# Performance work log

Measured on AMD Instinct MI355X. Metric: run time of the kernel, lower is better.

## Reference

```python
import jax, jax.numpy as jnp
import numpy as np

N_NODES = 20000
DEG = 6
E = N_NODES * DEG  # 120000 edges == line-graph nodes
D_NODE, D_EDGE = 64, 16
HID, OUT = 128, 128
EPS = 1e-5


def setup_inputs() -> dict:
    key = jax.random.key(0)
    ks = jax.random.split(key, 8)
    rng = np.random.default_rng(0)
    # graph: each node is the source of DEG edges (direction='out' -> index_r = edge_index[0])
    src = np.repeat(np.arange(N_NODES), DEG)
    dst = rng.integers(0, N_NODES, E)
    edge_index = np.stack([src, dst]).astype(np.int64)
    # two_step_index: ordered pairs of distinct edges sharing a source node
    # (bipartite 2-hop, self loops removed), then GATConv add_self_loops re-appends (i,i)
    ii, jj = np.meshgrid(np.arange(DEG), np.arange(DEG), indexing='ij')
    off = ~np.eye(DEG, dtype=bool)
    ii, jj = ii[off], jj[off]  # DEG*(DEG-1) within-group pairs
    base = (np.arange(N_NODES) * DEG)[:, None]
    s2 = np.concatenate([(base + ii[None, :]).ravel(), np.arange(E)])
    d2 = np.concatenate([(base + jj[None, :]).ravel(), np.arange(E)])
    index_2step = np.stack([s2, d2]).astype(np.int64)  # [2, 720000]
    d_in = D_NODE + D_EDGE
    return {
        "edge_attr": jax.random.normal(ks[0], (E, D_EDGE), jnp.float32),
        "node_attr": jax.random.normal(ks[1], (N_NODES, D_NODE), jnp.float32),
        "bn0_g": jnp.ones((d_in,), jnp.float32),
        "bn0_b": jnp.zeros((d_in,), jnp.float32),
        "W1": jax.random.normal(ks[2], (d_in, HID), jnp.float32) / np.sqrt(d_in).astype(np.float32),
        "bn1_g": jnp.ones((HID,), jnp.float32),
        "bn1_b": jnp.zeros((HID,), jnp.float32),
        "Wg": jax.random.normal(ks[3], (HID, OUT), jnp.float32) / np.sqrt(HID).astype(np.float32),
        "att_src": jax.random.normal(ks[4], (OUT,), jnp.float32) * 0.1,
        "att_dst": jax.random.normal(ks[5], (OUT,), jnp.float32) * 0.1,
        "gat_bias": jnp.zeros((OUT,), jnp.float32),
        "bnf_g": jnp.ones((OUT,), jnp.float32),
        "bnf_b": jnp.zeros((OUT,), jnp.float32),
        "edge_index": jnp.asarray(edge_index),
        "index_2step": jnp.asarray(index_2step),
        "num_nodes": N_NODES,
    }


def batch_norm(x, g, b):
    # training-mode BatchNorm1d (biased variance), like the torch module default
    mu = x.mean(0)
    var = x.var(0)
    return (x - mu) * jax.lax.rsqrt(var + EPS) * g + b


def reference(edge_attr, node_attr, bn0_g, bn0_b, W1, bn1_g, bn1_b,
              Wg, att_src, att_dst, gat_bias, bnf_g, bnf_b,
              edge_index, index_2step, num_nodes):
    index_r = edge_index[0]  # [E] source node of each edge (direction='out')
    # h0: per-edge concat of source-node attrs and edge attrs  [E, Dn+De]
    h0 = jnp.concatenate([node_attr[index_r], edge_attr], axis=1)
    # linear encoder: BN -> Linear(no bias) -> BN -> ReLU (dropout p=0)
    h1 = jax.nn.relu(batch_norm(batch_norm(h0, bn0_g, bn0_b) @ W1, bn1_g, bn1_b))
    # --- GATConv (heads=1) on the line graph given by index_2step ---
    E_ = h1.shape[0]
    x = h1 @ Wg                 # [E, OUT]
    a_src = x @ att_src         # [E]
    a_dst = x @ att_dst         # [E]
    s, d = index_2step[0], index_2step[1]
    e = jax.nn.leaky_relu(a_src[s] + a_dst[d], 0.2)          # [E2]
    e = e - jax.ops.segment_max(e, d, num_segments=E_)[d]    # stable edge-softmax
    ex = jnp.exp(e)
    alpha = ex / (jax.ops.segment_sum(ex, d, num_segments=E_)[d] + 1e-16)
    h2 = jax.ops.segment_sum(alpha[:, None] * x[s], d, num_segments=E_) + gat_bias
    # --- global_add_pool keyed by source node id, then final BatchNorm ---
    h3 = jax.ops.segment_sum(h2, index_r, num_segments=num_nodes)  # [N, OUT]
    return batch_norm(h3, bnf_g, bnf_b)
```

## Files before the change

kernel.cpp:

```cpp
#include <hip/hip_runtime.h>

#define N_NODES 20000
#define DEG 6
#define E_EDGES 120000
#define EPS_BN 1e-5f
#define NBLK 1250
#define EB 96
#define NB 16

#define WS_S0SUM 0
#define WS_S0SQ  80
#define WS_BIAS1 160
#define WS_S1SUM 288
#define WS_S1SQ  1312
#define WS_SC1M  2336
#define WS_SH1M  2464
#define WS_FSUM  2592
#define WS_FSQ   2720
#define WS_STATS_FLOATS 2848
#define WS_WT1   2848
#define WS_WGT   8992

typedef float f32x4 __attribute__((ext_vector_type(4)));
typedef short bf16x8 __attribute__((ext_vector_type(8)));

__device__ __forceinline__ unsigned short f2bf(float f) {
  unsigned u = __float_as_uint(f);
  u += 0x7fffu + ((u >> 16) & 1u);
  return (unsigned short)(u >> 16);
}
__device__ __forceinline__ unsigned pack2bf(float a, float b) {
  return (unsigned)f2bf(a) | ((unsigned)f2bf(b) << 16);
}

__global__ __launch_bounds__(256) void k1_bn0_stats(
    const float* __restrict__ node_attr, const float* __restrict__ edge_attr,
    float* __restrict__ ws) {
  __shared__ float red[256];
  const int t = threadIdx.x;
  const int b = blockIdx.x;
  if (b < 128) {
    const int c = t & 63, rl = t >> 6;
    float s = 0.f, q = 0.f;
    for (int row = b * 4 + rl; row < N_NODES; row += 512) {
      float v = node_attr[row * 64 + c];
      s += v; q += v * v;
    }
    red[t] = s;
    __syncthreads();
    if (t < 64) atomicAdd(&ws[WS_S0SUM + t], red[t] + red[t + 64] + red[t + 128] + red[t + 192]);
    __syncthreads();
    red[t] = q;
    __syncthreads();
    if (t < 64) atomicAdd(&ws[WS_S0SQ + t], red[t] + red[t + 64] + red[t + 128] + red[t + 192]);
  } else {
    const int c = t & 15, rl = t >> 4;
    float s = 0.f, q = 0.f;
    for (int row = (b - 128) * 16 + rl; row < E_EDGES; row += 2048) {
      float v = edge_attr[row * 16 + c];
      s += v; q += v * v;
    }
    red[t] = s;
    __syncthreads();
    if (t < 16) {
      float tot = 0.f;
      #pragma unroll
      for (int k = 0; k < 16; ++k) tot += red[t + 16 * k];
      atomicAdd(&ws[WS_S0SUM + 64 + t], tot);
    }
    __syncthreads();
    red[t] = q;
    __syncthreads();
    if (t < 16) {
      float tot = 0.f;
      #pragma unroll
      for (int k = 0; k < 16; ++k) tot += red[t + 16 * k];
      atomicAdd(&ws[WS_S0SQ + 64 + t], tot);
    }
  }
}

__global__ __launch_bounds__(256) void k0_fold(
    const float* __restrict__ W1, const float* __restrict__ Wg,
    const float* __restrict__ bn0_g, const float* __restrict__ bn0_b,
    float* __restrict__ ws) {
  short* wt1 = (short*)(ws + WS_WT1);
  short* wgt = (short*)(ws + WS_WGT);
  const int t0 = blockIdx.x * 256 + threadIdx.x;
  for (int i = t0; i < 128 * 96; i += 32 * 256) {
    int n = i / 96, k = i % 96;
    float v = 0.f;
    if (k < 80) {
      float cnt = (k < 64) ? (float)N_NODES : (float)E_EDGES;
      float mu = ws[WS_S0SUM + k] / cnt;
      float var = ws[WS_S0SQ + k] / cnt - mu * mu;
      v = W1[k * 128 + n] * (bn0_g[k] * rsqrtf(var + EPS_BN));
    }
    wt1[i] = (short)f2bf(v);
  }
  for (int i = t0; i < 128 * 128; i += 32 * 256) {
    int n = i >> 7, k = i & 127;
    wgt[i] = (short)f2bf(Wg[k * 128 + n]);
  }
  if (blockIdx.x == 0 && threadIdx.x < 128) {
    int n = threadIdx.x;
    float s = 0.f;
    for (int k = 0; k < 80; ++k) {
      float cnt = (k < 64) ? (float)N_NODES : (float)E_EDGES;
      float mu = ws[WS_S0SUM + k] / cnt;
      float var = ws[WS_S0SQ + k] / cnt - mu * mu;
      float sc = bn0_g[k] * rsqrtf(var + EPS_BN);
      s += (bn0_b[k] - mu * sc) * W1[k * 128 + n];
    }
    ws[WS_BIAS1 + n] = s;
  }
}

#define STAGE_INPUTS()                                                         \
  {                                                                            \
    int i = t;                                                                 \
    int row = i >> 4, c4 = (i & 15) << 2;                                      \
    float4 v = *(const float4*)&node_attr[(size_t)(g * NB + row) * 64 + c4];   \
    *(uint2*)&n0s[row * 72 + c4] = make_uint2(pack2bf(v.x, v.y), pack2bf(v.z, v.w)); \
  }                                                                            \
  for (int i = t; i < EB * 4; i += 256) {                                      \
    int row = i >> 2, c4 = (i & 3) << 2;                                       \
    float4 v = *(const float4*)&edge_attr[(size_t)(g * EB + row) * 16 + c4];   \
    *(uint2*)&e0s[row * 24 + c4] = make_uint2(pack2bf(v.x, v.y), pack2bf(v.z, v.w)); \
  }                                                                            \
  if (t < 8) zpad[t] = 0;

#define GEMM1_CORE(acc1)                                                       \
  _Pragma("unroll")                                                            \
  for (int ks = 0; ks < 3; ++ks) {                                             \
    bf16x8 bb0 = *(const bf16x8*)&wt1[(Nb + lm) * 96 + ks * 32 + lq * 8];      \
    bf16x8 bb1 = *(const bf16x8*)&wt1[(Nb + 16 + lm) * 96 + ks * 32 + lq * 8]; \
    _Pragma("unroll")                                                          \
    for (int mt = 0; mt < 6; ++mt) {                                           \
      const short* ap;                                                         \
      if (ks < 2) ap = &n0s[rowdiv6[mt] * 72 + ks * 32 + lq * 8];              \
      else ap = (lq < 2) ? &e0s[(mt * 16 + lm) * 24 + lq * 8] : zpad;          \
      bf16x8 a = *(const bf16x8*)ap;                                           \
      acc1[mt][0] = __builtin_amdgcn_mfma_f32_16x16x32_bf16(a, bb0, acc1[mt][0], 0, 0, 0); \
      acc1[mt][1] = __builtin_amdgcn_mfma_f32_16x16x32_bf16(a, bb1, acc1[mt][1], 0, 0, 0); \
    }                                                                          \
  }

__global__ __launch_bounds__(256, 2) void k2_bn1_stats(
    const float* __restrict__ node_attr, const float* __restrict__ edge_attr,
    float* __restrict__ ws) {
  __shared__ __align__(16) short n0s[16 * 72];
  __shared__ __align__(16) short e0s[96 * 24];
  __shared__ __align__(16) short zpad[8];
  const int t = threadIdx.x;
  const int g = blockIdx.x;
  const int l = t & 63, wid = t >> 6;
  const int lm = l & 15, lq = l >> 4;
  const int Nb = wid * 32;
  const short* wt1 = (const short*)(ws + WS_WT1);
  int rowdiv6[6];
  #pragma unroll
  for (int mt = 0; mt < 6; ++mt) rowdiv6[mt] = (mt * 16 + lm) / 6;
  float bias1c[2];
  bias1c[0] = ws[WS_BIAS1 + Nb + lm];
  bias1c[1] = ws[WS_BIAS1 + Nb + 16 + lm];
  STAGE_INPUTS();
  __syncthreads();
  f32x4 acc1[6][2] = {};
  GEMM1_CORE(acc1);
  const int set = g & 7;
  #pragma unroll
  for (int nt = 0; nt < 2; ++nt) {
    float s = 0.f, q = 0.f;
    #pragma unroll
    for (int mt = 0; mt < 6; ++mt)
      #pragma unroll
      for (int r = 0; r < 4; ++r) {
        float v = acc1[mt][nt][r] + bias1c[nt];
        s += v; q += v * v;
      }
    s += __shfl_xor(s, 16); s += __shfl_xor(s, 32);
    q += __shfl_xor(q, 16); q += __shfl_xor(q, 32);
    if (l < 16) {
      int col = Nb + nt * 16 + lm;
      atomicAdd(&ws[WS_S1SUM + set * 128 + col], s);
      atomicAdd(&ws[WS_S1SQ + set * 128 + col], q);
    }
  }
}

__global__ __launch_bounds__(128) void k2b_finalize(
    const float* __restrict__ bn1_g, const float* __restrict__ bn1_b,
    float* __restrict__ ws) {
  const int t = threadIdx.x;
  float s = 0.f, q = 0.f;
  #pragma unroll
  for (int st = 0; st < 8; ++st) {
    s += ws[WS_S1SUM + st * 128 + t];
    q += ws[WS_S1SQ + st * 128 + t];
  }
  const float invE = 1.f / (float)E_EDGES;
  float mu = s * invE;
  float var = q * invE - mu * mu;
  float sc1 = bn1_g[t] * rsqrtf(var + EPS_BN);
  float sh1 = bn1_b[t] - mu * sc1;
  ws[WS_SC1M + t] = sc1;
  ws[WS_SH1M + t] = ws[WS_BIAS1 + t] * sc1 + sh1;
}

__global__ __launch_bounds__(256, 2) void k3_fused(
    const float* __restrict__ node_attr, const float* __restrict__ edge_attr,
    const float* __restrict__ att_src, const float* __restrict__ att_dst,
    const float* __restrict__ gat_bias,
    float* __restrict__ out, float* __restrict__ ws) {
  __shared__ __align__(16) short n0s[16 * 72];
  __shared__ __align__(16) short e0s[96 * 24];
  __shared__ __align__(16) short zpad[8];
  __shared__ __align__(16) short h1s[96 * 136];
  __shared__ float asP[4][96], adP[4][96];
  __shared__ float asS[96], adS[96], wS[96];
  __shared__ float alphaL[96][6];
  __shared__ float h3L[16 * 128];

  const int t = threadIdx.x;
  const int g = blockIdx.x;
  const int l = t & 63, wid = t >> 6;
  const int lm = l & 15, lq = l >> 4;
  const int Nb = wid * 32;
  const short* wt1 = (const short*)(ws + WS_WT1);
  const short* wgt = (const short*)(ws + WS_WGT);
  int rowdiv6[6];
  #pragma unroll
  for (int mt = 0; mt < 6; ++mt) rowdiv6[mt] = (mt * 16 + lm) / 6;
  float sc1c[2], sh1c[2], atS[2], atD[2];
  #pragma unroll
  for (int nt = 0; nt < 2; ++nt) {
    int col = Nb + nt * 16 + lm;
    sc1c[nt] = ws[WS_SC1M + col];
    sh1c[nt] = ws[WS_SH1M + col];
    atS[nt] = att_src[col];
    atD[nt] = att_dst[col];
  }
  #pragma unroll
  for (int j = 0; j < 2; ++j)
    *(f32x4*)&h3L[(t + j * 256) * 4] = (f32x4){0.f, 0.f, 0.f, 0.f};
  STAGE_INPUTS();
  __syncthreads();
  {
    f32x4 acc1[6][2] = {};
    GEMM1_CORE(acc1);
    #pragma unroll
    for (int mt = 0; mt < 6; ++mt)
      #pragma unroll
      for (int nt = 0; nt < 2; ++nt)
        #pragma unroll
        for (int r = 0; r < 4; ++r) {
          int row = mt * 16 + lq * 4 + r;
          int col = Nb + nt * 16 + lm;
          float v = fmaxf(acc1[mt][nt][r] * sc1c[nt] + sh1c[nt], 0.f);
          h1s[row * 136 + col] = (short)f2bf(v);
        }
  }
  __syncthreads();
  f32x4 acc2[6][2] = {};
  #pragma unroll
  for (int ks = 0; ks < 4; ++ks) {
    bf16x8 bb0 = *(const bf16x8*)&wgt[(Nb + lm) * 128 + ks * 32 + lq * 8];
    bf16x8 bb1 = *(const bf16x8*)&wgt[(Nb + 16 + lm) * 128 + ks * 32 + lq * 8];
    #pragma unroll
    for (int mt = 0; mt < 6; ++mt) {
      bf16x8 a = *(const bf16x8*)&h1s[(mt * 16 + lm) * 136 + ks * 32 + lq * 8];
      acc2[mt][0] = __builtin_amdgcn_mfma_f32_16x16x32_bf16(a, bb0, acc2[mt][0], 0, 0, 0);
      acc2[mt][1] = __builtin_amdgcn_mfma_f32_16x16x32_bf16(a, bb1, acc2[mt][1], 0, 0, 0);
    }
  }
  {
    float ps, pd;
    #pragma unroll
    for (int mt = 0; mt < 6; ++mt)
      #pragma unroll
      for (int r = 0; r < 4; ++r) {
        ps = acc2[mt][0][r] * atS[0] + acc2[mt][1][r] * atS[1];
        pd = acc2[mt][0][r] * atD[0] + acc2[mt][1][r] * atD[1];
        #pragma unroll
        for (int off = 1; off < 16; off <<= 1) {
          ps += __shfl_xor(ps, off);
          pd += __shfl_xor(pd, off);
        }
        if (lm == 0) {
          int row = mt * 16 + lq * 4 + r;
          asP[wid][row] = ps;
          adP[wid][row] = pd;
        }
      }
  }
  __syncthreads();
  if (t < 96) {
    asS[t] = asP[0][t] + asP[1][t] + asP[2][t] + asP[3][t];
    adS[t] = adP[0][t] + adP[1][t] + adP[2][t] + adP[3][t];
  }
  __syncthreads();
  if (t < 96) {
    int n = t / 6;
    int nb6 = n * 6;
    float ad = adS[t];
    float s6[6], m = -1e30f;
    #pragma unroll
    for (int i = 0; i < 6; ++i) {
      float s = asS[nb6 + i] + ad;
      s = (s > 0.f) ? s : 0.2f * s;
      s6[i] = s; m = fmaxf(m, s);
    }
    float ssum = 0.f, ex[6];
    #pragma unroll
    for (int i = 0; i < 6; ++i) { ex[i] = __expf(s6[i] - m); ssum += ex[i]; }
    float inv = 1.f / (ssum + 1e-16f);
    #pragma unroll
    for (int i = 0; i < 6; ++i) alphaL[t][i] = ex[i] * inv;
  }
  __syncthreads();
  if (t < 96) {
    int n = t / 6, i = t % 6;
    float w = 0.f;
    #pragma unroll
    for (int j = 0; j < 6; ++j) w += alphaL[n * 6 + j][i];
    wS[t] = w;
  }
  __syncthreads();
  #pragma unroll
  for (int mt = 0; mt < 6; ++mt)
    #pragma unroll
    for (int r = 0; r < 4; ++r) {
      int row = mt * 16 + lq * 4 + r;
      float w = wS[row];
      int nl = row / 6;
      #pragma unroll
      for (int nt = 0; nt < 2; ++nt)
        atomicAdd(&h3L[nl * 128 + Nb + nt * 16 + lm], w * acc2[mt][nt][r]);
    }
  __syncthreads();
  #pragma unroll
  for (int j = 0; j < 2; ++j) {
    int idx = t + j * 256;
    int nslot = idx >> 5, c4 = (idx & 31) << 2;
    f32x4 v = *(f32x4*)&h3L[nslot * 128 + c4];
    const f32x4 gb = *(const f32x4*)&gat_bias[c4];
    v[0] += 6.f * gb[0]; v[1] += 6.f * gb[1];
    v[2] += 6.f * gb[2]; v[3] += 6.f * gb[3];
    *(f32x4*)&out[(size_t)(g * NB + nslot) * 128 + c4] = v;
  }
}

__global__ __launch_bounds__(256) void k4a_stats(
    const float* __restrict__ out, float* __restrict__ ws) {
  __shared__ float red[8][128];
  const int t = threadIdx.x;
  const int c4 = (t & 31) << 2, rl = t >> 5;
  float fs[4] = {0.f, 0.f, 0.f, 0.f}, fq[4] = {0.f, 0.f, 0.f, 0.f};
  for (int r = blockIdx.x * 8 + rl; r < N_NODES; r += 128 * 8) {
    float4 v = *(const float4*)&out[(size_t)r * 128 + c4];
    fs[0] += v.x; fq[0] += v.x * v.x;
    fs[1] += v.y; fq[1] += v.y * v.y;
    fs[2] += v.z; fq[2] += v.z * v.z;
    fs[3] += v.w; fq[3] += v.w * v.w;
  }
  #pragma unroll
  for (int j = 0; j < 4; ++j) red[rl][c4 + j] = fs[j];
  __syncthreads();
  if (t < 128) {
    float s = 0.f;
    #pragma unroll
    for (int k = 0; k < 8; ++k) s += red[k][t];
    atomicAdd(&ws[WS_FSUM + t], s);
  }
  __syncthreads();
  #pragma unroll
  for (int j = 0; j < 4; ++j) red[rl][c4 + j] = fq[j];
  __syncthreads();
  if (t < 128) {
    float s = 0.f;
    #pragma unroll
    for (int k = 0; k < 8; ++k) s += red[k][t];
    atomicAdd(&ws[WS_FSQ + t], s);
  }
}

__global__ __launch_bounds__(256) void k4b_apply(
    float* __restrict__ out, const float* __restrict__ ws,
    const float* __restrict__ bnf_g, const float* __restrict__ bnf_b) {
  int idx4 = blockIdx.x * 256 + threadIdx.x;
  if (idx4 >= N_NODES * 128 / 4) return;
  int c0 = (idx4 & 31) << 2;
  float4 v = ((float4*)out)[idx4];
  float4 fsv = *(const float4*)&ws[WS_FSUM + c0];
  float4 fqv = *(const float4*)&ws[WS_FSQ + c0];
  float4 g4 = *(const float4*)&bnf_g[c0];
  float4 b4 = *(const float4*)&bnf_b[c0];
  const float invN = 1.f / (float)N_NODES;
  float mu, var, sc;
  mu = fsv.x * invN; var = fqv.x * invN - mu * mu; sc = g4.x * rsqrtf(var + EPS_BN);
  v.x = (v.x - mu) * sc + b4.x;
  mu = fsv.y * invN; var = fqv.y * invN - mu * mu; sc = g4.y * rsqrtf(var + EPS_BN);
  v.y = (v.y - mu) * sc + b4.y;
  mu = fsv.z * invN; var = fqv.z * invN - mu * mu; sc = g4.z * rsqrtf(var + EPS_BN);
  v.z = (v.z - mu) * sc + b4.z;
  mu = fsv.w * invN; var = fqv.w * invN - mu * mu; sc = g4.w * rsqrtf(var + EPS_BN);
  v.w = (v.w - mu) * sc + b4.w;
  ((float4*)out)[idx4] = v;
}

extern "C" void kernel_launch(void* const* d_in, const int* in_sizes, int n_in,
                              void* d_out, int out_size, void* d_ws, size_t ws_size,
                              hipStream_t stream) {
  const float* edge_attr = (const float*)d_in[0];
  const float* node_attr = (const float*)d_in[1];
  const float* bn0_g = (const float*)d_in[2];
  const float* bn0_b = (const float*)d_in[3];
  const float* W1    = (const float*)d_in[4];
  const float* bn1_g = (const float*)d_in[5];
  const float* bn1_b = (const float*)d_in[6];
  const float* Wg    = (const float*)d_in[7];
  const float* att_src = (const float*)d_in[8];
  const float* att_dst = (const float*)d_in[9];
  const float* gat_bias = (const float*)d_in[10];
  const float* bnf_g = (const float*)d_in[11];
  const float* bnf_b = (const float*)d_in[12];
  float* ws = (float*)d_ws;
  float* out = (float*)d_out;

  hipMemsetAsync(d_ws, 0, WS_STATS_FLOATS * sizeof(float), stream);
  k1_bn0_stats<<<256, 256, 0, stream>>>(node_attr, edge_attr, ws);
  k0_fold<<<32, 256, 0, stream>>>(W1, Wg, bn0_g, bn0_b, ws);
  k2_bn1_stats<<<NBLK, 256, 0, stream>>>(node_attr, edge_attr, ws);
  k2b_finalize<<<1, 128, 0, stream>>>(bn1_g, bn1_b, ws);
  k3_fused<<<NBLK, 256, 0, stream>>>(node_attr, edge_attr, att_src, att_dst,
                                     gat_bias, out, ws);
  k4a_stats<<<128, 256, 0, stream>>>(out, ws);
  k4b_apply<<<2500, 256, 0, stream>>>(out, ws, bnf_g, bnf_b);
}
```

Measured before the change: 249.8 us.

## Fuse all stages into one persistent kernel with grid-wide barriers

Replaces the seven separate launches (BN0 stats, weight fold, BN1 stats, finalize, fused GAT, final stats, final apply) with a single persistent kernel of 512 blocks that loops over tiles. Stages are separated by a software grid barrier built on atomics. The intent is to remove per-launch overhead and inter-kernel gaps, and to fold the small finalize steps into per-block prologues. In exchange, every block redundantly recomputes the folded bf16 weights and the BN scales. The barrier also relies on all 512 blocks being co-resident, so it can deadlock if occupancy is lower than assumed.

```diff
diff --git a/kernel.cpp b/kernel.cpp
--- a/kernel.cpp
+++ b/kernel.cpp
@@ -4,22 +4,21 @@
 #define DEG 6
 #define E_EDGES 120000
 #define EPS_BN 1e-5f
-#define NBLK 1250
+#define NTILES 1250
 #define EB 96
 #define NB 16
-
-#define WS_S0SUM 0
-#define WS_S0SQ  80
-#define WS_BIAS1 160
-#define WS_S1SUM 288
-#define WS_S1SQ  1312
-#define WS_SC1M  2336
-#define WS_SH1M  2464
-#define WS_FSUM  2592
-#define WS_FSQ   2720
-#define WS_STATS_FLOATS 2848
-#define WS_WT1   2848
-#define WS_WGT   8992
+#define GRID 512
+
+#define WS_BAR   0
+#define WS_S0SUM 8
+#define WS_S0SQ  88
+#define WS_S1SUM 168
+#define WS_S1SQ  1192
+#define WS_FSUM  2216
+#define WS_FSQ   3240
+#define WS_STATS_FLOATS 4264
+#define WS_WT1   4264
+#define WS_WGT   10408
 
 typedef float f32x4 __attribute__((ext_vector_type(4)));
 typedef short bf16x8 __attribute__((ext_vector_type(8)));
@@ -33,87 +32,15 @@
   return (unsigned)f2bf(a) | ((unsigned)f2bf(b) << 16);
 }
 
-__global__ __launch_bounds__(256) void k1_bn0_stats(
-    const float* __restrict__ node_attr, const float* __restrict__ edge_attr,
-    float* __restrict__ ws) {
-  __shared__ float red[256];
-  const int t = threadIdx.x;
-  const int b = blockIdx.x;
-  if (b < 128) {
-    const int c = t & 63, rl = t >> 6;
-    float s = 0.f, q = 0.f;
-    for (int row = b * 4 + rl; row < N_NODES; row += 512) {
-      float v = node_attr[row * 64 + c];
-      s += v; q += v * v;
-    }
-    red[t] = s;
-    __syncthreads();
-    if (t < 64) atomicAdd(&ws[WS_S0SUM + t], red[t] + red[t + 64] + red[t + 128] + red[t + 192]);
-    __syncthreads();
-    red[t] = q;
-    __syncthreads();
-    if (t < 64) atomicAdd(&ws[WS_S0SQ + t], red[t] + red[t + 64] + red[t + 128] + red[t + 192]);
-  } else {
-    const int c = t & 15, rl = t >> 4;
-    float s = 0.f, q = 0.f;
-    for (int row = (b - 128) * 16 + rl; row < E_EDGES; row += 2048) {
-      float v = edge_attr[row * 16 + c];
-      s += v; q += v * v;
-    }
-    red[t] = s;
-    __syncthreads();
-    if (t < 16) {
-      float tot = 0.f;
-      #pragma unroll
-      for (int k = 0; k < 16; ++k) tot += red[t + 16 * k];
-      atomicAdd(&ws[WS_S0SUM + 64 + t], tot);
-    }
-    __syncthreads();
-    red[t] = q;
-    __syncthreads();
-    if (t < 16) {
-      float tot = 0.f;
-      #pragma unroll
-      for (int k = 0; k < 16; ++k) tot += red[t + 16 * k];
-      atomicAdd(&ws[WS_S0SQ + 64 + t], tot);
-    }
-  }
-}
-
-__global__ __launch_bounds__(256) void k0_fold(
-    const float* __restrict__ W1, const float* __restrict__ Wg,
-    const float* __restrict__ bn0_g, const float* __restrict__ bn0_b,
-    float* __restrict__ ws) {
-  short* wt1 = (short*)(ws + WS_WT1);
-  short* wgt = (short*)(ws + WS_WGT);
-  const int t0 = blockIdx.x * 256 + threadIdx.x;
-  for (int i = t0; i < 128 * 96; i += 32 * 256) {
-    int n = i / 96, k = i % 96;
-    float v = 0.f;
-    if (k < 80) {
-      float cnt = (k < 64) ? (float)N_NODES : (float)E_EDGES;
-      float mu = ws[WS_S0SUM + k] / cnt;
-      float var = ws[WS_S0SQ + k] / cnt - mu * mu;
-      v = W1[k * 128 + n] * (bn0_g[k] * rsqrtf(var + EPS_BN));
-    }
-    wt1[i] = (short)f2bf(v);
-  }
-  for (int i = t0; i < 128 * 128; i += 32 * 256) {
-    int n = i >> 7, k = i & 127;
-    wgt[i] = (short)f2bf(Wg[k * 128 + n]);
-  }
-  if (blockIdx.x == 0 && threadIdx.x < 128) {
-    int n = threadIdx.x;
-    float s = 0.f;
-    for (int k = 0; k < 80; ++k) {
-      float cnt = (k < 64) ? (float)N_NODES : (float)E_EDGES;
-      float mu = ws[WS_S0SUM + k] / cnt;
-      float var = ws[WS_S0SQ + k] / cnt - mu * mu;
-      float sc = bn0_g[k] * rsqrtf(var + EPS_BN);
-      s += (bn0_b[k] - mu * sc) * W1[k * 128 + n];
-    }
-    ws[WS_BIAS1 + n] = s;
-  }
+__device__ __forceinline__ void gbar(int* bar, int idx) {
+  __syncthreads();
+  if (threadIdx.x == 0) {
+    __threadfence();
+    atomicAdd(&bar[idx], 1);
+    while (atomicAdd(&bar[idx], 0) < GRID) __builtin_amdgcn_s_sleep(4);
+    __threadfence();
+  }
+  __syncthreads();
 }
 
 #define STAGE_INPUTS()                                                         \
@@ -146,142 +73,208 @@
     }                                                                          \
   }
 
-__global__ __launch_bounds__(256, 2) void k2_bn1_stats(
-    const float* __restrict__ node_attr, const float* __restrict__ edge_attr,
-    float* __restrict__ ws) {
-  __shared__ __align__(16) short n0s[16 * 72];
-  __shared__ __align__(16) short e0s[96 * 24];
-  __shared__ __align__(16) short zpad[8];
-  const int t = threadIdx.x;
-  const int g = blockIdx.x;
-  const int l = t & 63, wid = t >> 6;
-  const int lm = l & 15, lq = l >> 4;
-  const int Nb = wid * 32;
-  const short* wt1 = (const short*)(ws + WS_WT1);
-  int rowdiv6[6];
-  #pragma unroll
-  for (int mt = 0; mt < 6; ++mt) rowdiv6[mt] = (mt * 16 + lm) / 6;
-  float bias1c[2];
-  bias1c[0] = ws[WS_BIAS1 + Nb + lm];
-  bias1c[1] = ws[WS_BIAS1 + Nb + 16 + lm];
-  STAGE_INPUTS();
-  __syncthreads();
-  f32x4 acc1[6][2] = {};
-  GEMM1_CORE(acc1);
-  const int set = g & 7;
-  #pragma unroll
-  for (int nt = 0; nt < 2; ++nt) {
-    float s = 0.f, q = 0.f;
-    #pragma unroll
-    for (int mt = 0; mt < 6; ++mt)
-      #pragma unroll
-      for (int r = 0; r < 4; ++r) {
-        float v = acc1[mt][nt][r] + bias1c[nt];
-        s += v; q += v * v;
-      }
-    s += __shfl_xor(s, 16); s += __shfl_xor(s, 32);
-    q += __shfl_xor(q, 16); q += __shfl_xor(q, 32);
-    if (l < 16) {
-      int col = Nb + nt * 16 + lm;
-      atomicAdd(&ws[WS_S1SUM + set * 128 + col], s);
-      atomicAdd(&ws[WS_S1SQ + set * 128 + col], q);
-    }
-  }
-}
-
-__global__ __launch_bounds__(128) void k2b_finalize(
+__global__ __launch_bounds__(256, 2) void mega(
+    const float* __restrict__ edge_attr, const float* __restrict__ node_attr,
+    const float* __restrict__ bn0_g, const float* __restrict__ bn0_b,
+    const float* __restrict__ W1,
     const float* __restrict__ bn1_g, const float* __restrict__ bn1_b,
-    float* __restrict__ ws) {
-  const int t = threadIdx.x;
-  float s = 0.f, q = 0.f;
-  #pragma unroll
-  for (int st = 0; st < 8; ++st) {
-    s += ws[WS_S1SUM + st * 128 + t];
-    q += ws[WS_S1SQ + st * 128 + t];
-  }
-  const float invE = 1.f / (float)E_EDGES;
-  float mu = s * invE;
-  float var = q * invE - mu * mu;
-  float sc1 = bn1_g[t] * rsqrtf(var + EPS_BN);
-  float sh1 = bn1_b[t] - mu * sc1;
-  ws[WS_SC1M + t] = sc1;
-  ws[WS_SH1M + t] = ws[WS_BIAS1 + t] * sc1 + sh1;
-}
-
-__global__ __launch_bounds__(256, 2) void k3_fused(
-    const float* __restrict__ node_attr, const float* __restrict__ edge_attr,
+    const float* __restrict__ Wg,
     const float* __restrict__ att_src, const float* __restrict__ att_dst,
     const float* __restrict__ gat_bias,
+    const float* __restrict__ bnf_g, const float* __restrict__ bnf_b,
     float* __restrict__ out, float* __restrict__ ws) {
+  __shared__ float redS[256];
+  __shared__ float sc0L[80], sh0L[80];
+  __shared__ float bias1L[128];
   __shared__ __align__(16) short n0s[16 * 72];
   __shared__ __align__(16) short e0s[96 * 24];
   __shared__ __align__(16) short zpad[8];
   __shared__ __align__(16) short h1s[96 * 136];
   __shared__ float asP[4][96], adP[4][96];
-  __shared__ float asS[96], adS[96], wS[96];
+  __shared__ float asS[96], adS[96], wSm[96];
   __shared__ float alphaL[96][6];
   __shared__ float h3L[16 * 128];
+  __shared__ float bnfA[128], bnfB[128];
 
   const int t = threadIdx.x;
-  const int g = blockIdx.x;
+  const int b = blockIdx.x;
+  int* bar = (int*)ws;
+
+  if (b < 256) {
+    const int c = t & 63, rl = t >> 6;
+    float s = 0.f, q = 0.f;
+    for (int row = b * 4 + rl; row < N_NODES; row += 1024) {
+      float v = node_attr[row * 64 + c];
+      s += v; q += v * v;
+    }
+    redS[t] = s;
+    __syncthreads();
+    if (t < 64) atomicAdd(&ws[WS_S0SUM + t], redS[t] + redS[t + 64] + redS[t + 128] + redS[t + 192]);
+    __syncthreads();
+    redS[t] = q;
+    __syncthreads();
+    if (t < 64) atomicAdd(&ws[WS_S0SQ + t], redS[t] + redS[t + 64] + redS[t + 128] + redS[t + 192]);
+  } else {
+    const int c = t & 15, rl = t >> 4;
+    float s = 0.f, q = 0.f;
+    for (int row = (b - 256) * 16 + rl; row < E_EDGES; row += 4096) {
+      float v = edge_attr[row * 16 + c];
+      s += v; q += v * v;
+    }
+    redS[t] = s;
+    __syncthreads();
+    if (t < 16) {
+      float tot = 0.f;
+      #pragma unroll
+      for (int k = 0; k < 16; ++k) tot += redS[t + 16 * k];
+      atomicAdd(&ws[WS_S0SUM + 64 + t], tot);
+    }
+    __syncthreads();
+    redS[t] = q;
+    __syncthreads();
+    if (t < 16) {
+      float tot = 0.f;
+      #pragma unroll
+      for (int k = 0; k < 16; ++k) tot += redS[t + 16 * k];
+      atomicAdd(&ws[WS_S0SQ + 64 + t], tot);
+    }
+  }
+  gbar(bar, 0);
+
+  short* wt1 = (short*)(ws + WS_WT1);
+  short* wgt = (short*)(ws + WS_WGT);
+  if (t < 80) {
+    float cnt = (t < 64) ? (float)N_NODES : (float)E_EDGES;
+    float mu = ws[WS_S0SUM + t] / cnt;
+    float var = ws[WS_S0SQ + t] / cnt - mu * mu;
+    float sc = bn0_g[t] * rsqrtf(var + EPS_BN);
+    sc0L[t] = sc; sh0L[t] = bn0_b[t] - mu * sc;
+  }
+  __syncthreads();
+  for (int i = t; i < 128 * 96; i += 256) {
+    int n = i / 96, k = i % 96;
+    float v = (k < 80) ? W1[k * 128 + n] * sc0L[k] : 0.f;
+    wt1[i] = (short)f2bf(v);
+  }
+  for (int i = t; i < 128 * 128; i += 256) {
+    int n = i >> 7, k = i & 127;
+    wgt[i] = (short)f2bf(Wg[k * 128 + n]);
+  }
+  if (t < 128) {
+    float s = 0.f;
+    for (int k = 0; k < 80; ++k) s += sh0L[k] * W1[k * 128 + t];
+    bias1L[t] = s;
+  }
+  __syncthreads();
+
   const int l = t & 63, wid = t >> 6;
   const int lm = l & 15, lq = l >> 4;
   const int Nb = wid * 32;
-  const short* wt1 = (const short*)(ws + WS_WT1);
-  const short* wgt = (const short*)(ws + WS_WGT);
   int rowdiv6[6];
   #pragma unroll
   for (int mt = 0; mt < 6; ++mt) rowdiv6[mt] = (mt * 16 + lm) / 6;
+
+  {
+    float bias1c[2];
+    bias1c[0] = bias1L[Nb + lm];
+    bias1c[1] = bias1L[Nb + 16 + lm];
+    float s1[2] = {0.f, 0.f}, q1[2] = {0.f, 0.f};
+    for (int g = b; g < NTILES; g += GRID) {
+      __syncthreads();
+      STAGE_INPUTS();
+      __syncthreads();
+      f32x4 acc1[6][2] = {};
+      GEMM1_CORE(acc1);
+      #pragma unroll
+      for (int nt = 0; nt < 2; ++nt)
+        #pragma unroll
+        for (int mt = 0; mt < 6; ++mt)
+          #pragma unroll
+          for (int r = 0; r < 4; ++r) {
+            float v = acc1[mt][nt][r] + bias1c[nt];
+            s1[nt] += v; q1[nt] += v * v;
+          }
+    }
+    const int set = b & 7;
+    #pragma unroll
+    for (int nt = 0; nt < 2; ++nt) {
+      float s = s1[nt], q = q1[nt];
+      s += __shfl_xor(s, 16); s += __shfl_xor(s, 32);
+      q += __shfl_xor(q, 16); q += __shfl_xor(q, 32);
+      if (l < 16) {
+        int col = Nb + nt * 16 + lm;
+        atomicAdd(&ws[WS_S1SUM + set * 128 + col], s);
+        atomicAdd(&ws[WS_S1SQ + set * 128 + col], q);
+      }
+    }
+  }
+  gbar(bar, 1);
+
   float sc1c[2], sh1c[2], atS[2], atD[2];
   #pragma unroll
   for (int nt = 0; nt < 2; ++nt) {
     int col = Nb + nt * 16 + lm;
-    sc1c[nt] = ws[WS_SC1M + col];
-    sh1c[nt] = ws[WS_SH1M + col];
+    float s = 0.f, q = 0.f;
+    #pragma unroll
+    for (int st = 0; st < 8; ++st) {
+      s += ws[WS_S1SUM + st * 128 + col];
+      q += ws[WS_S1SQ + st * 128 + col];
+    }
+    const float invE = 1.f / (float)E_EDGES;
+    float mu = s * invE;
+    float var = q * invE - mu * mu;
+    float sc1 = bn1_g[col] * rsqrtf(var + EPS_BN);
+    float sh1 = bn1_b[col] - mu * sc1;
+    sc1c[nt] = sc1;
+    sh1c[nt] = bias1L[col] * sc1 + sh1;
     atS[nt] = att_src[col];
     atD[nt] = att_dst[col];
   }
-  #pragma unroll
-  for (int j = 0; j < 2; ++j)
-    *(f32x4*)&h3L[(t + j * 256) * 4] = (f32x4){0.f, 0.f, 0.f, 0.f};
-  STAGE_INPUTS();
-  __syncthreads();
-  {
-    f32x4 acc1[6][2] = {};
-    GEMM1_CORE(acc1);
+
+  const int c4 = (t & 31) * 4;
+  const f32x4 gb = *(const f32x4*)&gat_bias[c4];
+  float fsA[4] = {0.f, 0.f, 0.f, 0.f}, fqA[4] = {0.f, 0.f, 0.f, 0.f};
+  for (int g = b; g < NTILES; g += GRID) {
+    __syncthreads();
+    #pragma unroll
+    for (int j = 0; j < 2; ++j)
+      *(f32x4*)&h3L[(t + j * 256) * 4] = (f32x4){0.f, 0.f, 0.f, 0.f};
+    STAGE_INPUTS();
+    __syncthreads();
+    {
+      f32x4 acc1[6][2] = {};
+      GEMM1_CORE(acc1);
+      #pragma unroll
+      for (int mt = 0; mt < 6; ++mt)
+        #pragma unroll
+        for (int nt = 0; nt < 2; ++nt)
+          #pragma unroll
+          for (int r = 0; r < 4; ++r) {
+            int row = mt * 16 + lq * 4 + r;
+            int col = Nb + nt * 16 + lm;
+            float v = fmaxf(acc1[mt][nt][r] * sc1c[nt] + sh1c[nt], 0.f);
+            h1s[row * 136 + col] = (short)f2bf(v);
+          }
+    }
+    __syncthreads();
+    f32x4 acc2[6][2] = {};
+    #pragma unroll
+    for (int ks = 0; ks < 4; ++ks) {
+      bf16x8 bb0 = *(const bf16x8*)&wgt[(Nb + lm) * 128 + ks * 32 + lq * 8];
+      bf16x8 bb1 = *(const bf16x8*)&wgt[(Nb + 16 + lm) * 128 + ks * 32 + lq * 8];
+      #pragma unroll
+      for (int mt = 0; mt < 6; ++mt) {
+        bf16x8 a = *(const bf16x8*)&h1s[(mt * 16 + lm) * 136 + ks * 32 + lq * 8];
+        acc2[mt][0] = __builtin_amdgcn_mfma_f32_16x16x32_bf16(a, bb0, acc2[mt][0], 0, 0, 0);
+        acc2[mt][1] = __builtin_amdgcn_mfma_f32_16x16x32_bf16(a, bb1, acc2[mt][1], 0, 0, 0);
+      }
+    }
     #pragma unroll
     for (int mt = 0; mt < 6; ++mt)
       #pragma unroll
-      for (int nt = 0; nt < 2; ++nt)
-        #pragma unroll
-        for (int r = 0; r < 4; ++r) {
-          int row = mt * 16 + lq * 4 + r;
-          int col = Nb + nt * 16 + lm;
-          float v = fmaxf(acc1[mt][nt][r] * sc1c[nt] + sh1c[nt], 0.f);
-          h1s[row * 136 + col] = (short)f2bf(v);
-        }
-  }
-  __syncthreads();
-  f32x4 acc2[6][2] = {};
-  #pragma unroll
-  for (int ks = 0; ks < 4; ++ks) {
-    bf16x8 bb0 = *(const bf16x8*)&wgt[(Nb + lm) * 128 + ks * 32 + lq * 8];
-    bf16x8 bb1 = *(const bf16x8*)&wgt[(Nb + 16 + lm) * 128 + ks * 32 + lq * 8];
-    #pragma unroll
-    for (int mt = 0; mt < 6; ++mt) {
-      bf16x8 a = *(const bf16x8*)&h1s[(mt * 16 + lm) * 136 + ks * 32 + lq * 8];
-      acc2[mt][0] = __builtin_amdgcn_mfma_f32_16x16x32_bf16(a, bb0, acc2[mt][0], 0, 0, 0);
-      acc2[mt][1] = __builtin_amdgcn_mfma_f32_16x16x32_bf16(a, bb1, acc2[mt][1], 0, 0, 0);
-    }
-  }
-  {
-    float ps, pd;
-    #pragma unroll
-    for (int mt = 0; mt < 6; ++mt)
-      #pragma unroll
       for (int r = 0; r < 4; ++r) {
-        ps = acc2[mt][0][r] * atS[0] + acc2[mt][1][r] * atS[1];
-        pd = acc2[mt][0][r] * atD[0] + acc2[mt][1][r] * atD[1];
+        float ps = acc2[mt][0][r] * atS[0] + acc2[mt][1][r] * atS[1];
+        float pd = acc2[mt][0][r] * atD[0] + acc2[mt][1][r] * atD[1];
         #pragma unroll
         for (int off = 1; off < 16; off <<= 1) {
           ps += __shfl_xor(ps, off);
@@ -293,120 +286,111 @@
           adP[wid][row] = pd;
         }
       }
-  }
-  __syncthreads();
-  if (t < 96) {
-    asS[t] = asP[0][t] + asP[1][t] + asP[2][t] + asP[3][t];
-    adS[t] = adP[0][t] + adP[1][t] + adP[2][t] + adP[3][t];
-  }
-  __syncthreads();
-  if (t < 96) {
-    int n = t / 6;
-    int nb6 = n * 6;
-    float ad = adS[t];
-    float s6[6], m = -1e30f;
-    #pragma unroll
-    for (int i = 0; i < 6; ++i) {
-      float s = asS[nb6 + i] + ad;
-      s = (s > 0.f) ? s : 0.2f * s;
-      s6[i] = s; m = fmaxf(m, s);
-    }
-    float ssum = 0.f, ex[6];
-    #pragma unroll
-    for (int i = 0; i < 6; ++i) { ex[i] = __expf(s6[i] - m); ssum += ex[i]; }
-    float inv = 1.f / (ssum + 1e-16f);
-    #pragma unroll
-    for (int i = 0; i < 6; ++i) alphaL[t][i] = ex[i] * inv;
-  }
-  __syncthreads();
-  if (t < 96) {
-    int n = t / 6, i = t % 6;
-    float w = 0.f;
-    #pragma unroll
-    for (int j = 0; j < 6; ++j) w += alphaL[n * 6 + j][i];
-    wS[t] = w;
+    __syncthreads();
+    if (t < 96) {
+      asS[t] = asP[0][t] + asP[1][t] + asP[2][t] + asP[3][t];
+      adS[t] = adP[0][t] + adP[1][t] + adP[2][t] + adP[3][t];
+    }
+    __syncthreads();
+    if (t < 96) {
+      int n = t / 6, nb6 = n * 6;
+      float ad = adS[t];
+      float s6[6], m = -1e30f;
+      #pragma unroll
+      for (int i = 0; i < 6; ++i) {
+        float s = asS[nb6 + i] + ad;
+        s = (s > 0.f) ? s : 0.2f * s;
+        s6[i] = s; m = fmaxf(m, s);
+      }
+      float ssum = 0.f, ex[6];
+      #pragma unroll
+      for (int i = 0; i < 6; ++i) { ex[i] = __expf(s6[i] - m); ssum += ex[i]; }
+      float inv = 1.f / (ssum + 1e-16f);
+      #pragma unroll
+      for (int i = 0; i < 6; ++i) alphaL[t][i] = ex[i] * inv;
+    }
+    __syncthreads();
+    if (t < 96) {
+      int n = t / 6, i = t % 6;
+      float w = 0.f;
+      #pragma unroll
+      for (int j = 0; j < 6; ++j) w += alphaL[n * 6 + j][i];
+      wSm[t] = w;
+    }
+    __syncthreads();
+    #pragma unroll
+    for (int mt = 0; mt < 6; ++mt)
+      #pragma unroll
+      for (int r = 0; r < 4; ++r) {
+        int row = mt * 16 + lq * 4 + r;
+        float w = wSm[row];
+        int nl = row / 6;
+        #pragma unroll
+        for (int nt = 0; nt < 2; ++nt)
+          atomicAdd(&h3L[nl * 128 + Nb + nt * 16 + lm], w * acc2[mt][nt][r]);
+      }
+    __syncthreads();
+    #pragma unroll
+    for (int j = 0; j < 2; ++j) {
+      int idx = t + j * 256;
+      int nslot = idx >> 5;
+      f32x4 v = *(f32x4*)&h3L[nslot * 128 + c4];
+      v[0] += 6.f * gb[0]; v[1] += 6.f * gb[1];
+      v[2] += 6.f * gb[2]; v[3] += 6.f * gb[3];
+      *(f32x4*)&out[(size_t)(g * NB + nslot) * 128 + c4] = v;
+      #pragma unroll
+      for (int e = 0; e < 4; ++e) { fsA[e] += v[e]; fqA[e] += v[e] * v[e]; }
+    }
   }
   __syncthreads();
   #pragma unroll
-  for (int mt = 0; mt < 6; ++mt)
-    #pragma unroll
-    for (int r = 0; r < 4; ++r) {
-      int row = mt * 16 + lq * 4 + r;
-      float w = wS[row];
-      int nl = row / 6;
-      #pragma unroll
-      for (int nt = 0; nt < 2; ++nt)
-        atomicAdd(&h3L[nl * 128 + Nb + nt * 16 + lm], w * acc2[mt][nt][r]);
-    }
-  __syncthreads();
-  #pragma unroll
-  for (int j = 0; j < 2; ++j) {
-    int idx = t + j * 256;
-    int nslot = idx >> 5, c4 = (idx & 31) << 2;
-    f32x4 v = *(f32x4*)&h3L[nslot * 128 + c4];
-    const f32x4 gb = *(const f32x4*)&gat_bias[c4];
-    v[0] += 6.f * gb[0]; v[1] += 6.f * gb[1];
-    v[2] += 6.f * gb[2]; v[3] += 6.f * gb[3];
-    *(f32x4*)&out[(size_t)(g * NB + nslot) * 128 + c4] = v;
-  }
-}
-
-__global__ __launch_bounds__(256) void k4a_stats(
-    const float* __restrict__ out, float* __restrict__ ws) {
-  __shared__ float red[8][128];
-  const int t = threadIdx.x;
-  const int c4 = (t & 31) << 2, rl = t >> 5;
-  float fs[4] = {0.f, 0.f, 0.f, 0.f}, fq[4] = {0.f, 0.f, 0.f, 0.f};
-  for (int r = blockIdx.x * 8 + rl; r < N_NODES; r += 128 * 8) {
-    float4 v = *(const float4*)&out[(size_t)r * 128 + c4];
-    fs[0] += v.x; fq[0] += v.x * v.x;
-    fs[1] += v.y; fq[1] += v.y * v.y;
-    fs[2] += v.z; fq[2] += v.z * v.z;
-    fs[3] += v.w; fq[3] += v.w * v.w;
-  }
-  #pragma unroll
-  for (int j = 0; j < 4; ++j) red[rl][c4 + j] = fs[j];
+  for (int j = 0; j < 4; ++j) h3L[(t >> 5) * 128 + c4 + j] = fsA[j];
   __syncthreads();
   if (t < 128) {
     float s = 0.f;
     #pragma unroll
-    for (int k = 0; k < 8; ++k) s += red[k][t];
-    atomicAdd(&ws[WS_FSUM + t], s);
+    for (int k = 0; k < 8; ++k) s += h3L[k * 128 + t];
+    atomicAdd(&ws[WS_FSUM + (b & 7) * 128 + t], s);
   }
   __syncthreads();
   #pragma unroll
-  for (int j = 0; j < 4; ++j) red[rl][c4 + j] = fq[j];
+  for (int j = 0; j < 4; ++j) h3L[(t >> 5) * 128 + c4 + j] = fqA[j];
   __syncthreads();
   if (t < 128) {
     float s = 0.f;
     #pragma unroll
-    for (int k = 0; k < 8; ++k) s += red[k][t];
-    atomicAdd(&ws[WS_FSQ + t], s);
-  }
-}
-
-__global__ __launch_bounds__(256) void k4b_apply(
-    float* __restrict__ out, const float* __restrict__ ws,
-    const float* __restrict__ bnf_g, const float* __restrict__ bnf_b) {
-  int idx4 = blockIdx.x * 256 + threadIdx.x;
-  if (idx4 >= N_NODES * 128 / 4) return;
-  int c0 = (idx4 & 31) << 2;
-  float4 v = ((float4*)out)[idx4];
-  float4 fsv = *(const float4*)&ws[WS_FSUM + c0];
-  float4 fqv = *(const float4*)&ws[WS_FSQ + c0];
-  float4 g4 = *(const float4*)&bnf_g[c0];
-  float4 b4 = *(const float4*)&bnf_b[c0];
-  const float invN = 1.f / (float)N_NODES;
-  float mu, var, sc;
-  mu = fsv.x * invN; var = fqv.x * invN - mu * mu; sc = g4.x * rsqrtf(var + EPS_BN);
-  v.x = (v.x - mu) * sc + b4.x;
-  mu = fsv.y * invN; var = fqv.y * invN - mu * mu; sc = g4.y * rsqrtf(var + EPS_BN);
-  v.y = (v.y - mu) * sc + b4.y;
-  mu = fsv.z * invN; var = fqv.z * invN - mu * mu; sc = g4.z * rsqrtf(var + EPS_BN);
-  v.z = (v.z - mu) * sc + b4.z;
-  mu = fsv.w * invN; var = fqv.w * invN - mu * mu; sc = g4.w * rsqrtf(var + EPS_BN);
-  v.w = (v.w - mu) * sc + b4.w;
-  ((float4*)out)[idx4] = v;
+    for (int k = 0; k < 8; ++k) s += h3L[k * 128 + t];
+    atomicAdd(&ws[WS_FSQ + (b & 7) * 128 + t], s);
+  }
+  gbar(bar, 2);
+
+  if (t < 128) {
+    float s = 0.f, q = 0.f;
+    #pragma unroll
+    for (int st = 0; st < 8; ++st) {
+      s += ws[WS_FSUM + st * 128 + t];
+      q += ws[WS_FSQ + st * 128 + t];
+    }
+    const float invN = 1.f / (float)N_NODES;
+    float mu = s * invN;
+    float var = q * invN - mu * mu;
+    float sc = bnf_g[t] * rsqrtf(var + EPS_BN);
+    bnfA[t] = sc;
+    bnfB[t] = bnf_b[t] - mu * sc;
+  }
+  __syncthreads();
+  for (int g = b; g < NTILES; g += GRID) {
+    #pragma unroll
+    for (int j = 0; j < 2; ++j) {
+      int idx = t + j * 256;
+      int nslot = idx >> 5;
+      size_t off = (size_t)(g * NB + nslot) * 128 + c4;
+      f32x4 v = *(f32x4*)&out[off];
+      #pragma unroll
+      for (int e = 0; e < 4; ++e) v[e] = v[e] * bnfA[c4 + e] + bnfB[c4 + e];
+      *(f32x4*)&out[off] = v;
+    }
+  }
 }
 
 extern "C" void kernel_launch(void* const* d_in, const int* in_sizes, int n_in,
@@ -429,12 +413,7 @@
   float* out = (float*)d_out;
 
   hipMemsetAsync(d_ws, 0, WS_STATS_FLOATS * sizeof(float), stream);
-  k1_bn0_stats<<<256, 256, 0, stream>>>(node_attr, edge_attr, ws);
-  k0_fold<<<32, 256, 0, stream>>>(W1, Wg, bn0_g, bn0_b, ws);
-  k2_bn1_stats<<<NBLK, 256, 0, stream>>>(node_attr, edge_attr, ws);
-  k2b_finalize<<<1, 128, 0, stream>>>(bn1_g, bn1_b, ws);
-  k3_fused<<<NBLK, 256, 0, stream>>>(node_attr, edge_attr, att_src, att_dst,
-                                     gat_bias, out, ws);
-  k4a_stats<<<128, 256, 0, stream>>>(out, ws);
-  k4b_apply<<<2500, 256, 0, stream>>>(out, ws, bnf_g, bnf_b);
+  mega<<<GRID, 256, 0, stream>>>(edge_attr, node_attr, bn0_g, bn0_b, W1,
+                                 bn1_g, bn1_b, Wg, att_src, att_dst, gat_bias,
+                                 bnf_g, bnf_b, out, ws);
 }
```

Result: slower. 353.0 us (+41.3%).

## Halve per-block tile to 8 nodes and fuse softmax stages to raise occupancy

Applied to the files above, without the earlier changes.

Each block now handles 8 nodes (48 edges) instead of 16 (96), doubling the grid to 2500 blocks and raising launch_bounds occupancy from 2 to 6 blocks per SM. The softmax, alpha and column-sum steps are merged into one pass per thread, which recomputes the 6x6 softmax per thread but removes the alphaL shared array and two barriers. The goal is more resident waves to hide latency on the staging and MFMA phases and fewer synchronisations, at the cost of redundant exp work and reused weight loads amortised over fewer rows.

```diff
diff --git a/kernel.cpp b/kernel.cpp
--- a/kernel.cpp
+++ b/kernel.cpp
@@ -4,9 +4,9 @@
 #define DEG 6
 #define E_EDGES 120000
 #define EPS_BN 1e-5f
-#define NBLK 1250
-#define EB 96
-#define NB 16
+#define NBLK 2500
+#define EB 48
+#define NB 8
 
 #define WS_S0SUM 0
 #define WS_S0SQ  80
@@ -117,14 +117,13 @@
 }
 
 #define STAGE_INPUTS()                                                         \
-  {                                                                            \
-    int i = t;                                                                 \
-    int row = i >> 4, c4 = (i & 15) << 2;                                      \
+  if (t < NB * 16) {                                                           \
+    int row = t >> 4, c4 = (t & 15) << 2;                                      \
     float4 v = *(const float4*)&node_attr[(size_t)(g * NB + row) * 64 + c4];   \
     *(uint2*)&n0s[row * 72 + c4] = make_uint2(pack2bf(v.x, v.y), pack2bf(v.z, v.w)); \
   }                                                                            \
-  for (int i = t; i < EB * 4; i += 256) {                                      \
-    int row = i >> 2, c4 = (i & 3) << 2;                                       \
+  if (t < EB * 4) {                                                            \
+    int row = t >> 2, c4 = (t & 3) << 2;                                       \
     float4 v = *(const float4*)&edge_attr[(size_t)(g * EB + row) * 16 + c4];   \
     *(uint2*)&e0s[row * 24 + c4] = make_uint2(pack2bf(v.x, v.y), pack2bf(v.z, v.w)); \
   }                                                                            \
@@ -136,7 +135,7 @@
     bf16x8 bb0 = *(const bf16x8*)&wt1[(Nb + lm) * 96 + ks * 32 + lq * 8];      \
     bf16x8 bb1 = *(const bf16x8*)&wt1[(Nb + 16 + lm) * 96 + ks * 32 + lq * 8]; \
     _Pragma("unroll")                                                          \
-    for (int mt = 0; mt < 6; ++mt) {                                           \
+    for (int mt = 0; mt < 3; ++mt) {                                           \
       const short* ap;                                                         \
       if (ks < 2) ap = &n0s[rowdiv6[mt] * 72 + ks * 32 + lq * 8];              \
       else ap = (lq < 2) ? &e0s[(mt * 16 + lm) * 24 + lq * 8] : zpad;          \
@@ -146,11 +145,11 @@
     }                                                                          \
   }
 
-__global__ __launch_bounds__(256, 2) void k2_bn1_stats(
+__global__ __launch_bounds__(256, 6) void k2_bn1_stats(
     const float* __restrict__ node_attr, const float* __restrict__ edge_attr,
     float* __restrict__ ws) {
-  __shared__ __align__(16) short n0s[16 * 72];
-  __shared__ __align__(16) short e0s[96 * 24];
+  __shared__ __align__(16) short n0s[NB * 72];
+  __shared__ __align__(16) short e0s[EB * 24];
   __shared__ __align__(16) short zpad[8];
   const int t = threadIdx.x;
   const int g = blockIdx.x;
@@ -158,22 +157,22 @@
   const int lm = l & 15, lq = l >> 4;
   const int Nb = wid * 32;
   const short* wt1 = (const short*)(ws + WS_WT1);
-  int rowdiv6[6];
-  #pragma unroll
-  for (int mt = 0; mt < 6; ++mt) rowdiv6[mt] = (mt * 16 + lm) / 6;
+  int rowdiv6[3];
+  #pragma unroll
+  for (int mt = 0; mt < 3; ++mt) rowdiv6[mt] = (mt * 16 + lm) / 6;
   float bias1c[2];
   bias1c[0] = ws[WS_BIAS1 + Nb + lm];
   bias1c[1] = ws[WS_BIAS1 + Nb + 16 + lm];
   STAGE_INPUTS();
   __syncthreads();
-  f32x4 acc1[6][2] = {};
+  f32x4 acc1[3][2] = {};
   GEMM1_CORE(acc1);
   const int set = g & 7;
   #pragma unroll
   for (int nt = 0; nt < 2; ++nt) {
     float s = 0.f, q = 0.f;
     #pragma unroll
-    for (int mt = 0; mt < 6; ++mt)
+    for (int mt = 0; mt < 3; ++mt)
       #pragma unroll
       for (int r = 0; r < 4; ++r) {
         float v = acc1[mt][nt][r] + bias1c[nt];
@@ -208,19 +207,18 @@
   ws[WS_SH1M + t] = ws[WS_BIAS1 + t] * sc1 + sh1;
 }
 
-__global__ __launch_bounds__(256, 2) void k3_fused(
+__global__ __launch_bounds__(256, 6) void k3_fused(
     const float* __restrict__ node_attr, const float* __restrict__ edge_attr,
     const float* __restrict__ att_src, const float* __restrict__ att_dst,
     const float* __restrict__ gat_bias,
     float* __restrict__ out, float* __restrict__ ws) {
-  __shared__ __align__(16) short n0s[16 * 72];
-  __shared__ __align__(16) short e0s[96 * 24];
+  __shared__ __align__(16) short n0s[NB * 72];
+  __shared__ __align__(16) short e0s[EB * 24];
   __shared__ __align__(16) short zpad[8];
-  __shared__ __align__(16) short h1s[96 * 136];
-  __shared__ float asP[4][96], adP[4][96];
-  __shared__ float asS[96], adS[96], wS[96];
-  __shared__ float alphaL[96][6];
-  __shared__ float h3L[16 * 128];
+  __shared__ __align__(16) short h1s[EB * 136];
+  __shared__ float asP[4][EB], adP[4][EB];
+  __shared__ float asS[EB], adS[EB], wSm[EB];
+  __shared__ float h3L[NB * 128];
 
   const int t = threadIdx.x;
   const int g = blockIdx.x;
@@ -229,9 +227,9 @@
   const int Nb = wid * 32;
   const short* wt1 = (const short*)(ws + WS_WT1);
   const short* wgt = (const short*)(ws + WS_WGT);
-  int rowdiv6[6];
-  #pragma unroll
-  for (int mt = 0; mt < 6; ++mt) rowdiv6[mt] = (mt * 16 + lm) / 6;
+  int rowdiv6[3];
+  #pragma unroll
+  for (int mt = 0; mt < 3; ++mt) rowdiv6[mt] = (mt * 16 + lm) / 6;
   float sc1c[2], sh1c[2], atS[2], atD[2];
   #pragma unroll
   for (int nt = 0; nt < 2; ++nt) {
@@ -241,16 +239,14 @@
     atS[nt] = att_src[col];
     atD[nt] = att_dst[col];
   }
-  #pragma unroll
-  for (int j = 0; j < 2; ++j)
-    *(f32x4*)&h3L[(t + j * 256) * 4] = (f32x4){0.f, 0.f, 0.f, 0.f};
+  *(f32x4*)&h3L[t * 4] = (f32x4){0.f, 0.f, 0.f, 0.f};
   STAGE_INPUTS();
   __syncthreads();
   {
-    f32x4 acc1[6][2] = {};
+    f32x4 acc1[3][2] = {};
     GEMM1_CORE(acc1);
     #pragma unroll
-    for (int mt = 0; mt < 6; ++mt)
+    for (int mt = 0; mt < 3; ++mt)
       #pragma unroll
       for (int nt = 0; nt < 2; ++nt)
         #pragma unroll
@@ -262,87 +258,73 @@
         }
   }
   __syncthreads();
-  f32x4 acc2[6][2] = {};
+  f32x4 acc2[3][2] = {};
   #pragma unroll
   for (int ks = 0; ks < 4; ++ks) {
     bf16x8 bb0 = *(const bf16x8*)&wgt[(Nb + lm) * 128 + ks * 32 + lq * 8];
     bf16x8 bb1 = *(const bf16x8*)&wgt[(Nb + 16 + lm) * 128 + ks * 32 + lq * 8];
     #pragma unroll
-    for (int mt = 0; mt < 6; ++mt) {
+    for (int mt = 0; mt < 3; ++mt) {
       bf16x8 a = *(const bf16x8*)&h1s[(mt * 16 + lm) * 136 + ks * 32 + lq * 8];
       acc2[mt][0] = __builtin_amdgcn_mfma_f32_16x16x32_bf16(a, bb0, acc2[mt][0], 0, 0, 0);
       acc2[mt][1] = __builtin_amdgcn_mfma_f32_16x16x32_bf16(a, bb1, acc2[mt][1], 0, 0, 0);
     }
   }
-  {
-    float ps, pd;
-    #pragma unroll
-    for (int mt = 0; mt < 6; ++mt)
-      #pragma unroll
-      for (int r = 0; r < 4; ++r) {
-        ps = acc2[mt][0][r] * atS[0] + acc2[mt][1][r] * atS[1];
-        pd = acc2[mt][0][r] * atD[0] + acc2[mt][1][r] * atD[1];
-        #pragma unroll
-        for (int off = 1; off < 16; off <<= 1) {
-          ps += __shfl_xor(ps, off);
-          pd += __shfl_xor(pd, off);
-        }
-        if (lm == 0) {
-          int row = mt * 16 + lq * 4 + r;
-          asP[wid][row] = ps;
-          adP[wid][row] = pd;
-        }
+  #pragma unroll
+  for (int mt = 0; mt < 3; ++mt)
+    #pragma unroll
+    for (int r = 0; r < 4; ++r) {
+      float ps = acc2[mt][0][r] * atS[0] + acc2[mt][1][r] * atS[1];
+      float pd = acc2[mt][0][r] * atD[0] + acc2[mt][1][r] * atD[1];
+      #pragma unroll
+      for (int off = 1; off < 16; off <<= 1) {
+        ps += __shfl_xor(ps, off);
+        pd += __shfl_xor(pd, off);
       }
-  }
-  __syncthreads();
-  if (t < 96) {
+      if (lm == 0) {
+        int row = mt * 16 + lq * 4 + r;
+        asP[wid][row] = ps;
+        adP[wid][row] = pd;
+      }
+    }
+  __syncthreads();
+  if (t < EB) {
     asS[t] = asP[0][t] + asP[1][t] + asP[2][t] + asP[3][t];
     adS[t] = adP[0][t] + adP[1][t] + adP[2][t] + adP[3][t];
-  }
-  __syncthreads();
-  if (t < 96) {
-    int n = t / 6;
-    int nb6 = n * 6;
-    float ad = adS[t];
-    float s6[6], m = -1e30f;
-    #pragma unroll
-    for (int i = 0; i < 6; ++i) {
-      float s = asS[nb6 + i] + ad;
-      s = (s > 0.f) ? s : 0.2f * s;
-      s6[i] = s; m = fmaxf(m, s);
-    }
-    float ssum = 0.f, ex[6];
-    #pragma unroll
-    for (int i = 0; i < 6; ++i) { ex[i] = __expf(s6[i] - m); ssum += ex[i]; }
-    float inv = 1.f / (ssum + 1e-16f);
-    #pragma unroll
-    for (int i = 0; i < 6; ++i) alphaL[t][i] = ex[i] * inv;
-  }
-  __syncthreads();
-  if (t < 96) {
-    int n = t / 6, i = t % 6;
+    int n = t / 6, i = t % 6, nb6 = n * 6;
     float w = 0.f;
     #pragma unroll
-    for (int j = 0; j < 6; ++j) w += alphaL[n * 6 + j][i];
-    wS[t] = w;
-  }
-  __syncthreads();
-  #pragma unroll
-  for (int mt = 0; mt < 6; ++mt)
+    for (int j = 0; j < 6; ++j) {
+      float ad = adS[nb6 + j];
+      float e[6], m = -1e30f;
+      #pragma unroll
+      for (int s = 0; s < 6; ++s) {
+        float x = asS[nb6 + s] + ad;
+        x = (x > 0.f) ? x : 0.2f * x;
+        e[s] = x; m = fmaxf(m, x);
+      }
+      float den = 0.f;
+      #pragma unroll
+      for (int s = 0; s < 6; ++s) den += __expf(e[s] - m);
+      w += __expf(e[i] - m) / (den + 1e-16f);
+    }
+    wSm[t] = w;
+  }
+  __syncthreads();
+  #pragma unroll
+  for (int mt = 0; mt < 3; ++mt)
     #pragma unroll
     for (int r = 0; r < 4; ++r) {
       int row = mt * 16 + lq * 4 + r;
-      float w = wS[row];
+      float w = wSm[row];
       int nl = row / 6;
       #pragma unroll
       for (int nt = 0; nt < 2; ++nt)
         atomicAdd(&h3L[nl * 128 + Nb + nt * 16 + lm], w * acc2[mt][nt][r]);
     }
   __syncthreads();
-  #pragma unroll
-  for (int j = 0; j < 2; ++j) {
-    int idx = t + j * 256;
-    int nslot = idx >> 5, c4 = (idx & 31) << 2;
+  {
+    int nslot = t >> 5, c4 = (t & 31) << 2;
     f32x4 v = *(f32x4*)&h3L[nslot * 128 + c4];
     const f32x4 gb = *(const f32x4*)&gat_bias[c4];
     v[0] += 6.f * gb[0]; v[1] += 6.f * gb[1];
```

Measured after the change: 253.9 us. No clear change (+1.6%).
